# Kernel tuning notes

Hardware: AMD Instinct MI355X
Metric: run time of the kernel (lower is better)

The kernel has to match this reference:

```python
import jax, jax.numpy as jnp
import numpy as np

N = 100000        # nodes
E = 1600000       # edges (avg degree 16)
D = 9             # num_divisions
IN_F = 128
OUT_F = 64


def setup_inputs() -> dict:
    key = jax.random.key(0)
    k1, k2, k3, k4, k5, k6 = jax.random.split(key, 6)
    feature = jax.random.normal(k1, (N, IN_F), dtype=jnp.float32)
    norm = jax.random.uniform(k2, (N, 1), dtype=jnp.float32)
    # Xavier-uniform-ish per-division weights, stored as [D, out, in] (torch Linear layout)
    limit = float(np.sqrt(6.0 / (IN_F + OUT_F)))
    W = jax.random.uniform(k3, (D, OUT_F, IN_F), dtype=jnp.float32, minval=-limit, maxval=limit)
    src = jax.random.randint(k4, (E,), 0, N, dtype=jnp.int32)
    dst = jax.random.randint(k5, (E,), 0, N, dtype=jnp.int32)
    edge_div = jax.random.randint(k6, (E,), 0, D, dtype=jnp.int32)
    return {"feature": feature, "norm": norm, "W": W, "src": src, "dst": dst, "edge_div": edge_div}


def reference(feature, norm, W, src, dst, edge_div):
    # Per-division linear projection fused with source-node norm scaling.
    # Wh: [D, N, out] = for each division i: (feature @ W_i^T) * norm
    Wh = jnp.einsum('nf,dof->dno', feature, W) * norm[None, :, :]
    # copy_u + sum message passing restricted to each division's edge subgraph:
    # gather per-edge message from (division, src), scatter-add into (division, dst).
    msg = Wh[edge_div, src]                                  # [E, out]
    h = jnp.zeros((D, N, OUT_F), dtype=Wh.dtype).at[edge_div, dst].add(msg)
    # merge == 'cat': concatenate divisions along feature axis -> [N, D*out]
    h_cat = jnp.transpose(h, (1, 0, 2)).reshape(N, D * OUT_F)
    # destination-node norm scaling + activation (relu)
    return jax.nn.relu(h_cat * norm)
```

## Files before the change

### kernel.cpp

```cpp
#include <hip/hip_runtime.h>
#include <hip/hip_bf16.h>

#define NN    100000
#define EE    1600000
#define DD    9
#define INF   128
#define OUTF  64
#define DOUT  (DD * OUTF)

#define NB     196
#define SUB    8
#define CAPS   1280
#define CAPB   (SUB * CAPS)
#define P1_EPB 2048
#define P1_BLOCKS ((EE + P1_EPB - 1) / P1_EPB)

#define GEMM_BX     1563
#define GEMM_BLOCKS (GEMM_BX * 3)
#define MEGA_BLOCKS (7 * P1_BLOCKS)

typedef __bf16 bf16x8 __attribute__((ext_vector_type(8)));
typedef float  f32x4  __attribute__((ext_vector_type(4)));
typedef unsigned short us4 __attribute__((ext_vector_type(4)));
typedef unsigned short us8 __attribute__((ext_vector_type(8)));

__device__ __forceinline__ unsigned short f32_to_bf16_rne(float f) {
    unsigned int u = __float_as_uint(f);
    unsigned int r = u + 0x7FFFu + ((u >> 16) & 1u);
    return (unsigned short)(r >> 16);
}

__device__ __forceinline__ float bf16_to_f32(unsigned short h) {
    return __uint_as_float(((unsigned int)h) << 16);
}

__global__ __launch_bounds__(256) void cvt_bf16_kernel(
    const float* __restrict__ in, unsigned short* __restrict__ out, int n4,
    int* __restrict__ bcount)
{
    int i = blockIdx.x * 256 + threadIdx.x;
    if (i < n4) {
        float4 v = reinterpret_cast<const float4*>(in)[i];
        ushort4 o;
        o.x = f32_to_bf16_rne(v.x);
        o.y = f32_to_bf16_rne(v.y);
        o.z = f32_to_bf16_rne(v.z);
        o.w = f32_to_bf16_rne(v.w);
        reinterpret_cast<ushort4*>(out)[i] = o;
    }
    for (int z = i; z < NB * SUB * 32; z += 18432)
        bcount[z] = 0;
}

__global__ __launch_bounds__(256) void mega_kernel(
    const float* __restrict__ feature,
    const unsigned short* __restrict__ Wb,
    const float* __restrict__ norm,
    unsigned short* __restrict__ Wh,
    const int* __restrict__ src, const int* __restrict__ dst,
    const int* __restrict__ ediv,
    int* __restrict__ bcount, int* __restrict__ bpay)
{
    __shared__ unsigned short lds[64 * 136];

    const int q  = blockIdx.x / 7;
    const int r7 = blockIdx.x % 7;

    if (r7 == 0) {
        int* shist  = (int*)lds;
        int* sgbase = (int*)lds + 256;
        const int tid = threadIdx.x;
        const int s   = q & (SUB - 1);
        if (tid < NB) shist[tid] = 0;
        __syncthreads();

        int pkt[8]; int cbv[8]; int lr[8];
        #pragma unroll
        for (int i = 0; i < 8; ++i) {
            int e = q * P1_EPB + i * 256 + tid;
            if (e < EE) {
                int dn = dst[e];
                cbv[i] = dn >> 9;
                pkt[i] = ((dn & 511) << 21) | (src[e] << 4) | ediv[e];
                lr[i]  = atomicAdd(&shist[cbv[i]], 1);
            } else {
                cbv[i] = -1;
            }
        }
        __syncthreads();
        if (tid < NB) {
            int h = shist[tid];
            if (h > 0)
                sgbase[tid] = atomicAdd(&bcount[(tid * SUB + s) * 32], h);
        }
        __syncthreads();
        #pragma unroll
        for (int i = 0; i < 8; ++i) {
            if (cbv[i] >= 0) {
                int pos = sgbase[cbv[i]] + lr[i];
                if (pos < CAPS)
                    bpay[cbv[i] * CAPB + s * CAPS + pos] = pkt[i];
            }
        }
        return;
    }

    const int gid  = q * 6 + (r7 - 1);
    if (gid >= GEMM_BLOCKS) return;
    const int nb   = (gid % GEMM_BX) * 64;
    const int d0   = (gid / GEMM_BX) * 3;
    const int tid  = threadIdx.x;
    const int wv   = tid >> 6;
    const int lane = tid & 63;
    const int quad = lane >> 4;
    const int m16  = lane & 15;

    const float* fb = feature + (size_t)nb * INF;
    #pragma unroll
    for (int it = 0; it < 4; ++it) {
        int chunk = it * 256 + tid;
        int node = chunk >> 4;
        int seg  = chunk & 15;
        us8 o;
        if (nb + node < NN) {
            float nm = norm[nb + node];
            const float4* fp = reinterpret_cast<const float4*>(fb + (size_t)node * INF + seg * 8);
            float4 a = fp[0], b4 = fp[1];
            o[0] = f32_to_bf16_rne(a.x * nm);  o[1] = f32_to_bf16_rne(a.y * nm);
            o[2] = f32_to_bf16_rne(a.z * nm);  o[3] = f32_to_bf16_rne(a.w * nm);
            o[4] = f32_to_bf16_rne(b4.x * nm); o[5] = f32_to_bf16_rne(b4.y * nm);
            o[6] = f32_to_bf16_rne(b4.z * nm); o[7] = f32_to_bf16_rne(b4.w * nm);
        } else {
            o = us8{};
        }
        *reinterpret_cast<us8*>(&lds[node * 136 + seg * 8]) = o;
    }
    __syncthreads();

    bf16x8 bfrag[4];
    {
        const unsigned short* rp = &lds[(wv * 16 + m16) * 136 + quad * 8];
        #pragma unroll
        for (int k = 0; k < 4; ++k)
            bfrag[k] = *reinterpret_cast<const bf16x8*>(rp + k * 32);
    }
    __syncthreads();

    #pragma unroll
    for (int dd = 0; dd < 3; ++dd) {
        const int d = d0 + dd;
        const unsigned short* wbase = Wb + (size_t)d * OUTF * INF;
        f32x4 acc[4] = {f32x4{0,0,0,0}, f32x4{0,0,0,0}, f32x4{0,0,0,0}, f32x4{0,0,0,0}};
        #pragma unroll
        for (int k = 0; k < 4; ++k) {
            #pragma unroll
            for (int f = 0; f < 4; ++f) {
                const bf16x8 afrag = *reinterpret_cast<const bf16x8*>(
                    wbase + (size_t)(f * 16 + m16) * INF + k * 32 + quad * 8);
                acc[f] = __builtin_amdgcn_mfma_f32_16x16x32_bf16(afrag, bfrag[k], acc[f], 0, 0, 0);
            }
        }
        {
            unsigned short* sp = &lds[(wv * 16 + m16) * 72 + quad * 4];
            #pragma unroll
            for (int f = 0; f < 4; ++f) {
                us4 p;
                p[0] = f32_to_bf16_rne(acc[f][0]);
                p[1] = f32_to_bf16_rne(acc[f][1]);
                p[2] = f32_to_bf16_rne(acc[f][2]);
                p[3] = f32_to_bf16_rne(acc[f][3]);
                *reinterpret_cast<us4*>(sp + f * 16) = p;
            }
        }
        #pragma unroll
        for (int j = 0; j < 2; ++j) {
            int row = wv * 16 + j * 8 + (lane >> 3);
            int seg = lane & 7;
            us8 v = *reinterpret_cast<const us8*>(&lds[row * 72 + seg * 8]);
            int node = nb + row;
            if (node < NN)
                *reinterpret_cast<us8*>(Wh + (size_t)node * DOUT + d * OUTF + seg * 8) = v;
        }
    }
}

__global__ __launch_bounds__(256) void sort2_kernel(
    int* __restrict__ bpay, const int* __restrict__ bcount,
    int* __restrict__ nodebase, int* __restrict__ count)
{
    __shared__ int ebuf[CAPB];
    __shared__ int hist2[512], base2[512], rank2[512];
    const int cb  = blockIdx.x;
    const int tid = threadIdx.x;
    const int n0  = cb * 512;
    const int nn  = min(512, NN - n0);

    for (int j = tid; j < 512; j += 256) { hist2[j] = 0; rank2[j] = 0; }
    __syncthreads();

    int off = 0;
    #pragma unroll
    for (int s = 0; s < SUB; ++s) {
        int cs = min(bcount[(cb * SUB + s) * 32], CAPS);
        for (int e = tid; e < cs; e += 256) {
            int p = bpay[cb * CAPB + s * CAPS + e];
            ebuf[off + e] = p;
            atomicAdd(&hist2[(unsigned)p >> 21], 1);
        }
        off += cs;
    }
    const int cnt = off;
    __syncthreads();

    if (tid < 64) {
        int carry = 0;
        #pragma unroll
        for (int ch = 0; ch < 8; ++ch) {
            int idx = ch * 64 + tid;
            int v = hist2[idx];
            int sc = v;
            #pragma unroll
            for (int o = 1; o < 64; o <<= 1) {
                int t = __shfl_up(sc, o);
                if (tid >= o) sc += t;
            }
            base2[idx] = carry + sc - v;
            carry += __shfl(sc, 63);
        }
    }
    __syncthreads();

    for (int e = tid; e < cnt; e += 256) {
        int p = ebuf[e];
        int d = (unsigned)p >> 21;
        int lr = atomicAdd(&rank2[d], 1);
        bpay[cb * CAPB + base2[d] + lr] = p & 0x1FFFFF;
    }
    for (int j = tid; j < nn; j += 256) {
        nodebase[n0 + j] = cb * CAPB + base2[j];
        count[n0 + j] = hist2[j];
    }
}

__global__ __launch_bounds__(256) void gather_kernel(
    const unsigned short* __restrict__ Wh, const int* __restrict__ bpay,
    const int* __restrict__ nodebase, const int* __restrict__ count,
    const float* __restrict__ norm, float* __restrict__ out)
{
    const int wv   = threadIdx.x >> 6;
    const int lane = threadIdx.x & 63;
    const int n = blockIdx.x * 4 + wv;
    if (n >= NN) return;
    const int c = count[n];
    const int b = nodebase[n];

    float acc[DD];
    #pragma unroll
    for (int k = 0; k < DD; ++k) acc[k] = 0.0f;

    for (int i0 = 0; i0 < c; i0 += 64) {
        const int take = min(c - i0, 64);
        int pv = (lane < take) ? bpay[b + i0 + lane] : 15;
        for (int j = 0; j < take; j += 8) {
            float v[8];
            int   dv[8];
            #pragma unroll
            for (int u = 0; u < 8; ++u) {
                int p = __builtin_amdgcn_readlane(pv, min(j + u, 63));
                dv[u] = p & 15;
                v[u] = bf16_to_f32(Wh[(size_t)(p >> 4) * DOUT + dv[u] * OUTF + lane]);
            }
            #pragma unroll
            for (int u = 0; u < 8; ++u) {
                #pragma unroll
                for (int k = 0; k < DD; ++k) {
                    float m = (dv[u] == k) ? 1.0f : 0.0f;
                    acc[k] += m * v[u];
                }
            }
        }
    }

    const float nm = norm[n];
    #pragma unroll
    for (int k = 0; k < DD; ++k)
        out[(size_t)n * DOUT + k * OUTF + lane] = fmaxf(acc[k] * nm, 0.0f);
}

extern "C" void kernel_launch(void* const* d_in, const int* in_sizes, int n_in,
                              void* d_out, int out_size, void* d_ws, size_t ws_size,
                              hipStream_t stream) {
    const float* feature = (const float*)d_in[0];
    const float* norm    = (const float*)d_in[1];
    const float* W       = (const float*)d_in[2];
    const int*   src     = (const int*)d_in[3];
    const int*   dst     = (const int*)d_in[4];
    const int*   ediv    = (const int*)d_in[5];
    float* out = (float*)d_out;

    char* ws = (char*)d_ws;
    unsigned short* Wh = (unsigned short*)ws;
    int* count    = (int*)(ws + 115200000);
    int* nodebase = (int*)(ws + 115600000);
    int* bcount   = (int*)(ws + 116000000);
    int* bpay     = (int*)(ws + 116204800);
    unsigned short* Wb = (unsigned short*)(ws + 124300000);

    const int nw4 = DD * OUTF * INF / 4;
    cvt_bf16_kernel<<<(nw4 + 255) / 256, 256, 0, stream>>>(W, Wb, nw4, bcount);

    mega_kernel<<<MEGA_BLOCKS, 256, 0, stream>>>(
        feature, Wb, norm, Wh, src, dst, ediv, bcount, bpay);

    sort2_kernel<<<NB, 256, 0, stream>>>(bpay, bcount, nodebase, count);

    gather_kernel<<<(NN + 3) / 4, 256, 0, stream>>>(Wh, bpay, nodebase, count, norm, out);
}
```

Baseline: 505.3 us.

## Split fused edge-bucketing/GEMM mega kernel into separate bucketing and GEMM launches

Replaces the mega kernel, which interleaved edge-bucketing blocks with GEMM blocks in a single launch, with two kernels: a bucketing kernel with its own small LDS footprint and a GEMM kernel on a 2D grid. The bucketing kernel now issues all global loads before the LDS atomics, with a scheduling barrier between them, so memory latency overlaps. The aim is to stop the lightweight bucketing blocks from carrying the GEMM's large LDS allocation, which limits occupancy, and to remove the block-index divmod dispatch. In exchange the two phases no longer run concurrently and there is one more launch.

```diff
diff --git a/kernel.cpp b/kernel.cpp
--- a/kernel.cpp
+++ b/kernel.cpp
@@ -15,9 +15,7 @@
 #define P1_EPB 2048
 #define P1_BLOCKS ((EE + P1_EPB - 1) / P1_EPB)
 
-#define GEMM_BX     1563
-#define GEMM_BLOCKS (GEMM_BX * 3)
-#define MEGA_BLOCKS (7 * P1_BLOCKS)
+#define GEMM_BX 1563
 
 typedef __bf16 bf16x8 __attribute__((ext_vector_type(8)));
 typedef float  f32x4  __attribute__((ext_vector_type(4)));
@@ -52,63 +50,61 @@
         bcount[z] = 0;
 }
 
-__global__ __launch_bounds__(256) void mega_kernel(
+__global__ __launch_bounds__(256) void p1_kernel(
+    const int* __restrict__ src, const int* __restrict__ dst,
+    const int* __restrict__ ediv,
+    int* __restrict__ bcount, int* __restrict__ bpay)
+{
+    __shared__ int shist[NB];
+    __shared__ int sgbase[NB];
+    const int tid = threadIdx.x;
+    const int q   = blockIdx.x;
+    const int s   = q & (SUB - 1);
+    if (tid < NB) shist[tid] = 0;
+    __syncthreads();
+
+    int pkt[8]; int cbv[8]; int lr[8];
+    #pragma unroll
+    for (int i = 0; i < 8; ++i) {
+        int e = q * P1_EPB + i * 256 + tid;
+        if (e < EE) {
+            int dn = dst[e];
+            cbv[i] = dn >> 9;
+            pkt[i] = ((dn & 511) << 21) | (src[e] << 4) | ediv[e];
+        } else {
+            cbv[i] = -1;
+        }
+    }
+    __builtin_amdgcn_sched_barrier(0);
+    #pragma unroll
+    for (int i = 0; i < 8; ++i)
+        if (cbv[i] >= 0) lr[i] = atomicAdd(&shist[cbv[i]], 1);
+    __syncthreads();
+    if (tid < NB) {
+        int h = shist[tid];
+        if (h > 0)
+            sgbase[tid] = atomicAdd(&bcount[(tid * SUB + s) * 32], h);
+    }
+    __syncthreads();
+    #pragma unroll
+    for (int i = 0; i < 8; ++i) {
+        if (cbv[i] >= 0) {
+            int pos = sgbase[cbv[i]] + lr[i];
+            if (pos < CAPS)
+                bpay[cbv[i] * CAPB + s * CAPS + pos] = pkt[i];
+        }
+    }
+}
+
+__global__ __launch_bounds__(256) void gemm_wh_kernel(
     const float* __restrict__ feature,
     const unsigned short* __restrict__ Wb,
     const float* __restrict__ norm,
-    unsigned short* __restrict__ Wh,
-    const int* __restrict__ src, const int* __restrict__ dst,
-    const int* __restrict__ ediv,
-    int* __restrict__ bcount, int* __restrict__ bpay)
+    unsigned short* __restrict__ Wh)
 {
     __shared__ unsigned short lds[64 * 136];
-
-    const int q  = blockIdx.x / 7;
-    const int r7 = blockIdx.x % 7;
-
-    if (r7 == 0) {
-        int* shist  = (int*)lds;
-        int* sgbase = (int*)lds + 256;
-        const int tid = threadIdx.x;
-        const int s   = q & (SUB - 1);
-        if (tid < NB) shist[tid] = 0;
-        __syncthreads();
-
-        int pkt[8]; int cbv[8]; int lr[8];
-        #pragma unroll
-        for (int i = 0; i < 8; ++i) {
-            int e = q * P1_EPB + i * 256 + tid;
-            if (e < EE) {
-                int dn = dst[e];
-                cbv[i] = dn >> 9;
-                pkt[i] = ((dn & 511) << 21) | (src[e] << 4) | ediv[e];
-                lr[i]  = atomicAdd(&shist[cbv[i]], 1);
-            } else {
-                cbv[i] = -1;
-            }
-        }
-        __syncthreads();
-        if (tid < NB) {
-            int h = shist[tid];
-            if (h > 0)
-                sgbase[tid] = atomicAdd(&bcount[(tid * SUB + s) * 32], h);
-        }
-        __syncthreads();
-        #pragma unroll
-        for (int i = 0; i < 8; ++i) {
-            if (cbv[i] >= 0) {
-                int pos = sgbase[cbv[i]] + lr[i];
-                if (pos < CAPS)
-                    bpay[cbv[i] * CAPB + s * CAPS + pos] = pkt[i];
-            }
-        }
-        return;
-    }
-
-    const int gid  = q * 6 + (r7 - 1);
-    if (gid >= GEMM_BLOCKS) return;
-    const int nb   = (gid % GEMM_BX) * 64;
-    const int d0   = (gid / GEMM_BX) * 3;
+    const int nb   = blockIdx.x * 64;
+    const int d0   = blockIdx.y * 3;
     const int tid  = threadIdx.x;
     const int wv   = tid >> 6;
     const int lane = tid & 63;
@@ -309,8 +305,10 @@
     const int nw4 = DD * OUTF * INF / 4;
     cvt_bf16_kernel<<<(nw4 + 255) / 256, 256, 0, stream>>>(W, Wb, nw4, bcount);
 
-    mega_kernel<<<MEGA_BLOCKS, 256, 0, stream>>>(
-        feature, Wb, norm, Wh, src, dst, ediv, bcount, bpay);
+    p1_kernel<<<P1_BLOCKS, 256, 0, stream>>>(src, dst, ediv, bcount, bpay);
+
+    dim3 g1(GEMM_BX, 3);
+    gemm_wh_kernel<<<g1, 256, 0, stream>>>(feature, Wb, norm, Wh);
 
     sort2_kernel<<<NB, 256, 0, stream>>>(bpay, bcount, nodebase, count);
 
```

Measured after the change: 517.7 us. 1.02x slower.
